# Performance work log

Measured on AMD Instinct MI355X. Metric: run time of the kernel, lower is better.

Reference implementation:

```python
import jax, jax.numpy as jnp
import numpy as np

N = 50000      # nodes
E = 600000     # edges
F_ATOM = 78
D = 128        # hidden_dim = heads * head_dim
H = 8
C = D // H     # 16
ED = 12        # edge_dim
L = 4          # num_layers
B = 512        # graphs in batch
DFF = 4 * D
SCALE = 1.0 / float(np.sqrt(C))


def setup_inputs() -> dict:
    key = jax.random.key(0)
    ks = iter(jax.random.split(key, 128))
    rn = lambda s, sc=0.05: jax.random.normal(next(ks), s, jnp.float32) * sc
    inp = {
        "x": jax.random.normal(next(ks), (N, F_ATOM), jnp.float32),
        "edge_attr": jax.random.normal(next(ks), (E, ED), jnp.float32),
        "edge_index": jax.random.randint(next(ks), (2, E), 0, N),
        "batch": jnp.sort(jax.random.randint(next(ks), (N,), 0, B)),
        "Wemb": rn((F_ATOM, D)), "bemb": jnp.zeros((D,), jnp.float32),
        "Wout": rn((D, D)), "bout": jnp.zeros((D,), jnp.float32),
    }
    def stk(s, sc=0.05):
        return jnp.stack([rn(s, sc) for _ in range(L)])
    inp.update(
        Wq=stk((D, D)), bq=jnp.zeros((L, D), jnp.float32),
        Wk=stk((D, D)), bk=jnp.zeros((L, D), jnp.float32),
        Wv=stk((D, D)), bv=jnp.zeros((L, D), jnp.float32),
        We=stk((ED, D)), be=jnp.zeros((L, D), jnp.float32),
        Wskip=stk((D, D)), bskip=jnp.zeros((L, D), jnp.float32),
        Wbeta=stk((3 * D,)),
        g1=jnp.ones((L, D), jnp.float32), b1=jnp.zeros((L, D), jnp.float32),
        g2=jnp.ones((L, D), jnp.float32), b2=jnp.zeros((L, D), jnp.float32),
        Wf1=stk((D, DFF)), bf1=jnp.zeros((L, DFF), jnp.float32),
        Wf2=stk((DFF, D)), bf2=jnp.zeros((L, D), jnp.float32),
    )
    return inp


def _ln(x, g, b):
    mu = jnp.mean(x, -1, keepdims=True)
    var = jnp.mean((x - mu) ** 2, -1, keepdims=True)
    return (x - mu) * jax.lax.rsqrt(var + 1e-5) * g + b


def _seg_softmax(alpha, dst):
    # alpha: [E, H]; softmax over edges sharing a destination node
    m = jax.ops.segment_max(alpha, dst, num_segments=N)
    m = jnp.where(jnp.isfinite(m), m, 0.0)
    ex = jnp.exp(alpha - m[dst])
    den = jax.ops.segment_sum(ex, dst, num_segments=N)
    return ex / (den[dst] + 1e-16)


def _forward(x, edge_attr, Wemb, bemb, Wq, bq, Wk, bk, Wv, bv, We, be,
             Wskip, bskip, Wbeta, g1, b1, g2, b2, Wf1, bf1, Wf2, bf2,
             Wout, bout, edge_index, batch):
    src, dst = edge_index[0], edge_index[1]
    h = x @ Wemb + bemb                                    # [N, D]
    for l in range(L):
        q = (h @ Wq[l] + bq[l]).reshape(N, H, C)
        k = (h @ Wk[l] + bk[l]).reshape(N, H, C)
        v = (h @ Wv[l] + bv[l]).reshape(N, H, C)
        e = (edge_attr @ We[l] + be[l]).reshape(E, H, C)
        kj = k[src] + e                                    # [E, H, C]
        alpha = jnp.einsum('ehc,ehc->eh', q[dst], kj) * SCALE
        a = _seg_softmax(alpha, dst)                       # [E, H]
        msg = (v[src] + e) * a[:, :, None]                 # [E, H, C]
        agg = jax.ops.segment_sum(msg, dst, num_segments=N).reshape(N, D)
        xr = h @ Wskip[l] + bskip[l]                       # root/skip transform
        beta = jax.nn.sigmoid(
            jnp.concatenate([agg, xr, agg - xr], -1) @ Wbeta[l])[:, None]
        hc = beta * xr + (1.0 - beta) * agg                # beta gate
        h = _ln(hc + h, g1[l], b1[l])
        ff = jax.nn.relu(h @ Wf1[l] + bf1[l]) @ Wf2[l] + bf2[l]
        h = _ln(ff + h, g2[l], b2[l])
    cnt = jax.ops.segment_sum(jnp.ones((N,), h.dtype), batch, num_segments=B)
    pooled = jax.ops.segment_sum(h, batch, num_segments=B) / jnp.maximum(cnt, 1.0)[:, None]
    return pooled @ Wout + bout                            # [B, D]


def reference(x, edge_attr, edge_index, batch, Wemb, bemb, Wout, bout,
              Wq, bq, Wk, bk, Wv, bv, We, be, Wskip, bskip, Wbeta,
              g1, b1, g2, b2, Wf1, bf1, Wf2, bf2):
    return _forward(x, edge_attr, Wemb, bemb, Wq, bq, Wk, bk, Wv, bv, We, be,
                    Wskip, bskip, Wbeta, g1, b1, g2, b2, Wf1, bf1, Wf2, bf2,
                    Wout, bout, edge_index, batch)
```

## Files before the change

### kernel.cpp

```cpp
#include <hip/hip_runtime.h>
#include <math.h>

#define N_NODES 50000
#define N_EDGES 600000
#define FATOM   78
#define DIM     128
#define HEADS   8
#define EDIM    12
#define LAYERS  4
#define NBATCH  512
#define NDFF    512
#define ASCALE  0.25f

typedef __attribute__((ext_vector_type(8))) short bf16x8;
typedef __attribute__((ext_vector_type(4))) float f32x4;

__device__ __forceinline__ float sum16(float v){
  #pragma unroll
  for (int m=1;m<16;m<<=1) v += __shfl_xor(v, m);
  return v;
}
__device__ __forceinline__ float half_sum(float v){
  #pragma unroll
  for (int m=1;m<32;m<<=1) v += __shfl_xor(v, m);
  return v;
}
__device__ __forceinline__ short f2b(float f){
  unsigned int u = __builtin_bit_cast(unsigned int, f);
  u += 0x7fffu + ((u>>16)&1u);
  return (short)(u>>16);
}
__device__ __forceinline__ float b2f_lo(unsigned int u){ return __builtin_bit_cast(float, u<<16); }
__device__ __forceinline__ float b2f_hi(unsigned int u){ return __builtin_bit_cast(float, u & 0xffff0000u); }

__device__ __forceinline__ void gload16(const short* g, short* l){
  __builtin_amdgcn_global_load_lds(
      (const __attribute__((address_space(1))) void*)g,
      (__attribute__((address_space(3))) void*)l, 16, 0, 0);
}

__global__ void count_kernel(const int* __restrict__ ei, int* __restrict__ cnt){
  int e = blockIdx.x*256 + threadIdx.x;
  if (e < N_EDGES) atomicAdd(&cnt[ei[N_EDGES + e]], 1);
}

__global__ __launch_bounds__(1024) void scan1(const int* __restrict__ cnt,
                                              int* __restrict__ row_start, int* __restrict__ bsum){
  __shared__ int lds[1024];
  int gid = blockIdx.x*1024 + threadIdx.x;
  int v = (gid < N_NODES) ? cnt[gid] : 0;
  lds[threadIdx.x] = v; __syncthreads();
  for (int off=1; off<1024; off<<=1){
    int add = (threadIdx.x>=off)?lds[threadIdx.x-off]:0;
    __syncthreads();
    lds[threadIdx.x]+=add;
    __syncthreads();
  }
  if (gid < N_NODES) row_start[gid+1] = lds[threadIdx.x];
  if (threadIdx.x==1023) bsum[blockIdx.x] = lds[1023];
}
__global__ void scan2(int* __restrict__ bsum, int nb){
  int tid = threadIdx.x;
  int v = (tid < nb) ? bsum[tid] : 0;
  #pragma unroll
  for (int off=1; off<64; off<<=1){
    int u = __shfl_up(v, off);
    if (tid >= off) v += u;
  }
  if (tid < nb) bsum[tid] = v;
}
__global__ void scan3(int* __restrict__ row_start, const int* __restrict__ bsum){
  int gid = blockIdx.x*256 + threadIdx.x;
  if (gid == 0) row_start[0] = 0;
  if (gid < N_NODES){
    int blk = gid >> 10;
    if (blk > 0) row_start[gid+1] += bsum[blk-1];
  }
}

__global__ void scatter_kernel(const int* __restrict__ ei, const float* __restrict__ ea,
                               int* __restrict__ cnt2, const int* __restrict__ row_start,
                               int* __restrict__ src_s, short* __restrict__ ea_s){
  int e = blockIdx.x*256 + threadIdx.x;
  if (e < N_EDGES){
    int d = ei[N_EDGES + e];
    int pos = atomicAdd(&cnt2[d], 1);
    int p = row_start[d] + pos;
    src_s[p] = ei[e];
    const float* src = ea + (size_t)e*EDIM;
    unsigned int* dst = (unsigned int*)(ea_s + (size_t)p*EDIM);
    #pragma unroll
    for (int j=0;j<6;j++){
      unsigned int lo = (unsigned int)(unsigned short)f2b(src[2*j]);
      unsigned int hi = (unsigned int)(unsigned short)f2b(src[2*j+1]);
      dst[j] = lo | (hi<<16);
    }
  }
}

__global__ __launch_bounds__(256) void deg_hist(const int* __restrict__ cnt, int* __restrict__ dhist){
  __shared__ int lh[256];
  lh[threadIdx.x] = 0; __syncthreads();
  int n = blockIdx.x*256 + threadIdx.x;
  if (n < N_NODES){
    int d = cnt[n]; if (d > 255) d = 255;
    atomicAdd(&lh[d], 1);
  }
  __syncthreads();
  int c = lh[threadIdx.x];
  if (c) atomicAdd(&dhist[threadIdx.x], c);
}
__global__ __launch_bounds__(256) void deg_scan(const int* __restrict__ dhist, int* __restrict__ dstart){
  __shared__ int l[256];
  int t = threadIdx.x;
  int v = dhist[t];
  l[t] = v; __syncthreads();
  for (int off=1; off<256; off<<=1){
    int add = (t>=off)? l[t-off]:0;
    __syncthreads();
    l[t]+=add;
    __syncthreads();
  }
  dstart[t] = l[t]-v;
}
__global__ __launch_bounds__(256) void deg_place(const int* __restrict__ cnt, int* __restrict__ dcnt,
                                                 const int* __restrict__ dstart, int* __restrict__ perm){
  __shared__ int lh[256];
  __shared__ int lbase[256];
  __shared__ int lrank[256];
  int t = threadIdx.x;
  lh[t] = 0; lrank[t] = 0; __syncthreads();
  int n = blockIdx.x*256 + t;
  int d = -1;
  if (n < N_NODES){
    d = cnt[n]; if (d > 255) d = 255;
    atomicAdd(&lh[d], 1);
  }
  __syncthreads();
  int c = lh[t];
  lbase[t] = c ? atomicAdd(&dcnt[t], c) : 0;
  __syncthreads();
  if (n < N_NODES){
    int r = atomicAdd(&lrank[d], 1);
    perm[dstart[d] + lbase[d] + r] = n;
  }
}

__global__ __launch_bounds__(256) void pack_weights(
  const float* __restrict__ Wq, const float* __restrict__ Wk,
  const float* __restrict__ Wv, const float* __restrict__ Ws,
  const float* __restrict__ bq, const float* __restrict__ bk,
  const float* __restrict__ bv, const float* __restrict__ bs,
  const float* __restrict__ Wf1, const float* __restrict__ Wf2,
  short* __restrict__ wq_t, short* __restrict__ wf1_t, short* __restrict__ wf2_t,
  float* __restrict__ bqkvs)
{
  int l = blockIdx.y;
  int idx = blockIdx.x*256 + threadIdx.x;
  int sec = idx >> 16, r = idx & 65535;
  if (sec == 0){
    int n = r >> 7, k = r & 127;
    const float* W = (n<128)?Wq:(n<256)?Wk:(n<384)?Wv:Ws;
    float v = W[(size_t)l*16384 + k*128 + (n&127)];
    wq_t[(size_t)l*65536 + n*128 + k] = f2b(v);
    if (k == 0){
      const float* bb = (n<128)?bq:(n<256)?bk:(n<384)?bv:bs;
      bqkvs[l*512 + n] = bb[l*128 + (n&127)];
    }
  } else if (sec == 1){
    int n = r >> 7, k = r & 127;
    wf1_t[(size_t)l*65536 + n*128 + k] = f2b(Wf1[(size_t)l*65536 + k*512 + n]);
  } else {
    int n = r >> 9, k = r & 511;
    wf2_t[(size_t)l*65536 + n*512 + k] = f2b(Wf2[(size_t)l*65536 + k*128 + n]);
  }
}

__global__ void pack_emb(const float* __restrict__ Wemb, short* __restrict__ wemb_t){
  int idx = blockIdx.x*256 + threadIdx.x;
  int nn = idx >> 7, k = idx & 127;
  wemb_t[nn*128 + k] = (k < FATOM) ? f2b(Wemb[(size_t)k*DIM + nn]) : (short)0;
}

__global__ void cast_pad_x(const float* __restrict__ x, short* __restrict__ xb){
  int idx = blockIdx.x*256 + threadIdx.x;
  int n = idx >> 6, kp = (idx & 63)*2;
  if (n >= N_NODES) return;
  float v0 = (kp   < FATOM) ? x[(size_t)n*FATOM + kp]   : 0.f;
  float v1 = (kp+1 < FATOM) ? x[(size_t)n*FATOM + kp+1] : 0.f;
  unsigned int lo = (unsigned int)(unsigned short)f2b(v0);
  unsigned int hi = (unsigned int)(unsigned short)f2b(v1);
  *(unsigned int*)(xb + (size_t)n*128 + kp) = lo | (hi<<16);
}

__global__ __launch_bounds__(256) void mfma_gemm(
    const short* __restrict__ A,
    const short* __restrict__ Bt,
    const float* __restrict__ bias,
    float* __restrict__ Cf,
    short* __restrict__ Cb,
    int Nrows, int K, int M, int relu)
{
  __shared__ short As[128*64];
  __shared__ short Bs[128*64];
  int tid  = threadIdx.x;
  int lane = tid & 63;
  int wave = tid >> 6;
  int wr = wave >> 1, wc = wave & 1;
  int bm = blockIdx.x * 128, bn = blockIdx.y * 128;

  f32x4 zero = {0.f,0.f,0.f,0.f};
  f32x4 acc[4][4];
  #pragma unroll
  for (int m=0;m<4;m++)
    #pragma unroll
    for (int n=0;n<4;n++) acc[m][n] = zero;

  int r0 = wave*32;
  for (int k0 = 0; k0 < K; k0 += 64){
    #pragma unroll
    for (int it=0; it<4; ++it){
      int rr = r0 + it*8;
      int r  = rr + (lane>>3);
      int oct = (lane&7) ^ (r&7);
      int gr = bm + r; if (gr >= Nrows) gr = Nrows-1;
      gload16(A  + (size_t)gr*K       + k0 + oct*8, As + rr*64);
      gload16(Bt + (size_t)(bn + r)*K + k0 + oct*8, Bs + rr*64);
    }
    __syncthreads();
    #pragma unroll
    for (int ks=0; ks<2; ++ks){
      bf16x8 af[4], bfv[4];
      #pragma unroll
      for (int m=0;m<4;m++){
        int row = wr*64 + m*16 + (lane&15);
        int oi  = ks*4 + (lane>>4);
        af[m] = *(const bf16x8*)(As + row*64 + ((oi ^ (row&7))<<3));
      }
      #pragma unroll
      for (int n=0;n<4;n++){
        int col = wc*64 + n*16 + (lane&15);
        int oi  = ks*4 + (lane>>4);
        bfv[n] = *(const bf16x8*)(Bs + col*64 + ((oi ^ (col&7))<<3));
      }
      #pragma unroll
      for (int m=0;m<4;m++)
        #pragma unroll
        for (int n=0;n<4;n++)
          acc[m][n] = __builtin_amdgcn_mfma_f32_16x16x32_bf16(af[m], bfv[n], acc[m][n], 0, 0, 0);
    }
    __syncthreads();
  }

  #pragma unroll
  for (int m=0;m<4;m++){
    #pragma unroll
    for (int n=0;n<4;n++){
      int col = bn + wc*64 + n*16 + (lane&15);
      float bval = bias[col];
      #pragma unroll
      for (int j=0;j<4;j++){
        int row = bm + wr*64 + m*16 + (lane>>4)*4 + j;
        if (row < Nrows){
          float v = acc[m][n][j] + bval;
          if (relu) v = fmaxf(v, 0.f);
          if (Cf) Cf[(size_t)row*M + col] = v;
          if (Cb) Cb[(size_t)row*M + col] = f2b(v);
        }
      }
    }
  }
}

__global__ __launch_bounds__(256) void edge_attn_fused(
  const short* __restrict__ qkvx,
  const short* __restrict__ ea_s, const int* __restrict__ src_s,
  const float* __restrict__ Wel, const float* __restrict__ bel,
  const int* __restrict__ row_start, const int* __restrict__ perm,
  float* __restrict__ h, short* __restrict__ hb,
  const float* __restrict__ Wb, const float* __restrict__ g, const float* __restrict__ b)
{
  int wid = (blockIdx.x*256 + threadIdx.x) >> 4;
  if (wid >= N_NODES) return;
  int node = perm[wid];
  int ln = threadIdx.x & 15;
  int c0 = ln*8;

  const short* qrow = qkvx + (size_t)node*512;
  uint4 qu = *(const uint4*)(qrow + c0);
  float q0=b2f_lo(qu.x), q1=b2f_hi(qu.x), q2=b2f_lo(qu.y), q3=b2f_hi(qu.y);
  float q4=b2f_lo(qu.z), q5=b2f_hi(qu.z), q6=b2f_lo(qu.w), q7=b2f_hi(qu.w);

  float u[12];
  #pragma unroll
  for (int j=0;j<12;j++){
    float4 wA = *(const float4*)(Wel + j*DIM + c0);
    float4 wB = *(const float4*)(Wel + j*DIM + c0 + 4);
    float pp = q0*wA.x+q1*wA.y+q2*wA.z+q3*wA.w
             + q4*wB.x+q5*wB.y+q6*wB.z+q7*wB.w;
    u[j] = pp + __shfl_xor(pp,1);
  }
  float4 beA = *(const float4*)(bel + c0);
  float4 beB = *(const float4*)(bel + c0 + 4);
  float qbe;
  { float pp = q0*beA.x+q1*beA.y+q2*beA.z+q3*beA.w
             + q4*beB.x+q5*beB.y+q6*beB.z+q7*beB.w;
    qbe = pp + __shfl_xor(pp,1); }

  int rs = row_start[node], re = row_start[node+1];
  float den = 0.f;
  float av[8] = {0.f,0.f,0.f,0.f,0.f,0.f,0.f,0.f};
  float aEA[12] = {0.f,0.f,0.f,0.f,0.f,0.f,0.f,0.f,0.f,0.f,0.f,0.f};
  for (int i=rs; i<re; ++i){
    int s = src_s[i];
    const short* eap = ea_s + (size_t)i*EDIM;
    uint2 eu0 = *(const uint2*)(eap);
    uint2 eu1 = *(const uint2*)(eap+4);
    uint2 eu2 = *(const uint2*)(eap+8);
    float ea[12];
    ea[0]=b2f_lo(eu0.x); ea[1]=b2f_hi(eu0.x); ea[2]=b2f_lo(eu0.y); ea[3]=b2f_hi(eu0.y);
    ea[4]=b2f_lo(eu1.x); ea[5]=b2f_hi(eu1.x); ea[6]=b2f_lo(eu1.y); ea[7]=b2f_hi(eu1.y);
    ea[8]=b2f_lo(eu2.x); ea[9]=b2f_hi(eu2.x); ea[10]=b2f_lo(eu2.y); ea[11]=b2f_hi(eu2.y);
    const short* srow = qkvx + (size_t)s*512;
    uint4 ku = *(const uint4*)(srow + 128 + c0);
    uint4 vu = *(const uint4*)(srow + 256 + c0);
    float pp = q0*b2f_lo(ku.x) + q1*b2f_hi(ku.x) + q2*b2f_lo(ku.y) + q3*b2f_hi(ku.y)
             + q4*b2f_lo(ku.z) + q5*b2f_hi(ku.z) + q6*b2f_lo(ku.w) + q7*b2f_hi(ku.w);
    float alpha = pp + __shfl_xor(pp,1) + qbe;
    #pragma unroll
    for (int j=0;j<12;j++) alpha += ea[j]*u[j];
    float p = __expf(alpha * ASCALE);
    den += p;
    av[0] += p*b2f_lo(vu.x); av[1] += p*b2f_hi(vu.x);
    av[2] += p*b2f_lo(vu.y); av[3] += p*b2f_hi(vu.y);
    av[4] += p*b2f_lo(vu.z); av[5] += p*b2f_hi(vu.z);
    av[6] += p*b2f_lo(vu.w); av[7] += p*b2f_hi(vu.w);
    #pragma unroll
    for (int j=0;j<12;j++) aEA[j] += p*ea[j];
  }
  float inv = 1.f/(den + 1e-16f);
  float gg[8];
  #pragma unroll
  for (int c=0;c<8;c++) gg[c] = av[c]*inv;
  #pragma unroll
  for (int j=0;j<12;j++){
    float wgt = aEA[j]*inv;
    float4 wA = *(const float4*)(Wel + j*DIM + c0);
    float4 wB = *(const float4*)(Wel + j*DIM + c0 + 4);
    gg[0]+=wgt*wA.x; gg[1]+=wgt*wA.y; gg[2]+=wgt*wA.z; gg[3]+=wgt*wA.w;
    gg[4]+=wgt*wB.x; gg[5]+=wgt*wB.y; gg[6]+=wgt*wB.z; gg[7]+=wgt*wB.w;
  }
  gg[0]+=beA.x; gg[1]+=beA.y; gg[2]+=beA.z; gg[3]+=beA.w;
  gg[4]+=beB.x; gg[5]+=beB.y; gg[6]+=beB.z; gg[7]+=beB.w;

  uint4 xu = *(const uint4*)(qrow + 384 + c0);
  float x[8];
  x[0]=b2f_lo(xu.x); x[1]=b2f_hi(xu.x); x[2]=b2f_lo(xu.y); x[3]=b2f_hi(xu.y);
  x[4]=b2f_lo(xu.z); x[5]=b2f_hi(xu.z); x[6]=b2f_lo(xu.w); x[7]=b2f_hi(xu.w);
  float4 hA = *(const float4*)(h + (size_t)node*DIM + c0);
  float4 hB = *(const float4*)(h + (size_t)node*DIM + c0 + 4);
  float hv[8] = {hA.x,hA.y,hA.z,hA.w,hB.x,hB.y,hB.z,hB.w};
  float4 waA = *(const float4*)(Wb + c0),       waB = *(const float4*)(Wb + c0 + 4);
  float4 wxA = *(const float4*)(Wb + DIM + c0), wxB = *(const float4*)(Wb + DIM + c0 + 4);
  float4 wdA = *(const float4*)(Wb + 2*DIM + c0), wdB = *(const float4*)(Wb + 2*DIM + c0 + 4);
  float wa[8] = {waA.x,waA.y,waA.z,waA.w,waB.x,waB.y,waB.z,waB.w};
  float wx[8] = {wxA.x,wxA.y,wxA.z,wxA.w,wxB.x,wxB.y,wxB.z,wxB.w};
  float wd[8] = {wdA.x,wdA.y,wdA.z,wdA.w,wdB.x,wdB.y,wdB.z,wdB.w};
  float sacc = 0.f;
  #pragma unroll
  for (int c=0;c<8;c++) sacc += gg[c]*wa[c] + x[c]*wx[c] + (gg[c]-x[c])*wd[c];
  sacc = sum16(sacc);
  float beta = 1.f/(1.f + __expf(-sacc));
  float t[8], ts = 0.f;
  #pragma unroll
  for (int c=0;c<8;c++){ t[c] = beta*x[c] + (1.f-beta)*gg[c] + hv[c]; ts += t[c]; }
  float mu = sum16(ts)*(1.f/128.f);
  float vs = 0.f;
  #pragma unroll
  for (int c=0;c<8;c++){ t[c] -= mu; vs += t[c]*t[c]; }
  float var = sum16(vs)*(1.f/128.f);
  float r = rsqrtf(var + 1e-5f);
  float4 gA = *(const float4*)(g + c0), gB = *(const float4*)(g + c0 + 4);
  float4 bA = *(const float4*)(b + c0), bB = *(const float4*)(b + c0 + 4);
  float gv[8] = {gA.x,gA.y,gA.z,gA.w,gB.x,gB.y,gB.z,gB.w};
  float bv[8] = {bA.x,bA.y,bA.z,bA.w,bB.x,bB.y,bB.z,bB.w};
  float o[8];
  #pragma unroll
  for (int c=0;c<8;c++) o[c] = t[c]*r*gv[c] + bv[c];
  float4 oA = {o[0],o[1],o[2],o[3]}, oB = {o[4],o[5],o[6],o[7]};
  *(float4*)(h + (size_t)node*DIM + c0)     = oA;
  *(float4*)(h + (size_t)node*DIM + c0 + 4) = oB;
  uint4 ou;
  ou.x = (unsigned int)(unsigned short)f2b(o[0]) | ((unsigned int)(unsigned short)f2b(o[1])<<16);
  ou.y = (unsigned int)(unsigned short)f2b(o[2]) | ((unsigned int)(unsigned short)f2b(o[3])<<16);
  ou.z = (unsigned int)(unsigned short)f2b(o[4]) | ((unsigned int)(unsigned short)f2b(o[5])<<16);
  ou.w = (unsigned int)(unsigned short)f2b(o[6]) | ((unsigned int)(unsigned short)f2b(o[7])<<16);
  *(uint4*)(hb + (size_t)node*DIM + c0) = ou;
}

__global__ __launch_bounds__(256) void add_ln_kernel(
  const float* __restrict__ t_in, float* __restrict__ h, short* __restrict__ hb,
  const float* __restrict__ g, const float* __restrict__ b)
{
  int wid = (blockIdx.x*256 + threadIdx.x) >> 5;
  if (wid >= N_NODES) return;
  int ln = threadIdx.x & 31;
  int c0 = ln*4;
  float4 t2 = *(const float4*)(t_in + (size_t)wid*DIM + c0);
  float4 h2 = *(const float4*)(h    + (size_t)wid*DIM + c0);
  float t0=t2.x+h2.x, t1=t2.y+h2.y, t3v=t2.z+h2.z, t4=t2.w+h2.w;
  float mu = half_sum(t0+t1+t3v+t4)*(1.f/128.f);
  float d0=t0-mu, d1=t1-mu, d2=t3v-mu, d3=t4-mu;
  float var = half_sum(d0*d0+d1*d1+d2*d2+d3*d3)*(1.f/128.f);
  float r = rsqrtf(var + 1e-5f);
  float4 gv = *(const float4*)(g+c0);
  float4 bv = *(const float4*)(b+c0);
  float o0=d0*r*gv.x+bv.x, o1=d1*r*gv.y+bv.y, o2=d2*r*gv.z+bv.z, o3=d3*r*gv.w+bv.w;
  float4 o; o.x=o0; o.y=o1; o.z=o2; o.w=o3;
  *(float4*)(h + (size_t)wid*DIM + c0) = o;
  unsigned int u0 = (unsigned int)(unsigned short)f2b(o0) | ((unsigned int)(unsigned short)f2b(o1)<<16);
  unsigned int u1 = (unsigned int)(unsigned short)f2b(o2) | ((unsigned int)(unsigned short)f2b(o3)<<16);
  uint2 ou; ou.x=u0; ou.y=u1;
  *(uint2*)(hb + (size_t)wid*DIM + c0) = ou;
}

__global__ __launch_bounds__(128) void pool_out(
  const float* __restrict__ h, const int* __restrict__ batch,
  const float* __restrict__ Wout, const float* __restrict__ bout,
  float* __restrict__ out)
{
  int bidx = blockIdx.x;
  int d = threadIdx.x;
  __shared__ int seg[2];
  __shared__ float p[DIM];
  if (d < 2){
    int target = bidx + d;
    int lo = 0, hi = N_NODES;
    while (lo < hi){ int mid = (lo+hi)>>1; if (batch[mid] < target) lo = mid+1; else hi = mid; }
    seg[d] = lo;
  }
  __syncthreads();
  int lo = seg[0], hi = seg[1];
  float s = 0.f;
  for (int n=lo; n<hi; ++n) s += h[(size_t)n*DIM + d];
  float cnt = (float)(hi - lo);
  p[d] = s / fmaxf(cnt, 1.f);
  __syncthreads();
  float o = bout[d];
  #pragma unroll 8
  for (int kk=0; kk<DIM; ++kk) o += p[kk]*Wout[kk*DIM + d];
  out[bidx*DIM + d] = o;
}

extern "C" void kernel_launch(void* const* d_in, const int* in_sizes, int n_in,
                              void* d_out, int out_size, void* d_ws, size_t ws_size,
                              hipStream_t stream)
{
  const float* x     = (const float*)d_in[0];
  const float* ea    = (const float*)d_in[1];
  const int*   ei    = (const int*)d_in[2];
  const int*   batch = (const int*)d_in[3];
  const float* Wemb  = (const float*)d_in[4];
  const float* bemb  = (const float*)d_in[5];
  const float* Wout  = (const float*)d_in[6];
  const float* bout  = (const float*)d_in[7];
  const float* Wq    = (const float*)d_in[8];
  const float* bq    = (const float*)d_in[9];
  const float* Wk    = (const float*)d_in[10];
  const float* bk    = (const float*)d_in[11];
  const float* Wv    = (const float*)d_in[12];
  const float* bv    = (const float*)d_in[13];
  const float* We    = (const float*)d_in[14];
  const float* be    = (const float*)d_in[15];
  const float* Wskip = (const float*)d_in[16];
  const float* bskip = (const float*)d_in[17];
  const float* Wbeta = (const float*)d_in[18];
  const float* g1    = (const float*)d_in[19];
  const float* b1    = (const float*)d_in[20];
  const float* g2    = (const float*)d_in[21];
  const float* b2    = (const float*)d_in[22];
  const float* Wf1   = (const float*)d_in[23];
  const float* bf1   = (const float*)d_in[24];
  const float* Wf2   = (const float*)d_in[25];
  const float* bf2   = (const float*)d_in[26];
  float* out = (float*)d_out;

  float* ws     = (float*)d_ws;
  float* h      = ws;
  float* ffout  = h + (size_t)N_NODES*DIM;
  float* bqkvs  = ffout + (size_t)N_NODES*DIM;
  short* ea_s   = (short*)(bqkvs + LAYERS*512);
  short* hb     = ea_s + (size_t)N_EDGES*EDIM;
  short* region = hb + (size_t)N_NODES*DIM;
  short* xb     = region + (size_t)N_NODES*NDFF;
  short* wemb_t = xb + (size_t)N_NODES*DIM;
  short* wq_t   = wemb_t + DIM*DIM;
  short* wf1_t  = wq_t  + (size_t)LAYERS*NDFF*DIM;
  short* wf2_t  = wf1_t + (size_t)LAYERS*NDFF*DIM;
  int*   cnt       = (int*)(wf2_t + (size_t)LAYERS*NDFF*DIM);
  int*   cnt2      = cnt + N_NODES;
  int*   row_start = cnt2 + N_NODES;
  int*   bsum      = row_start + N_NODES + 1;
  int*   dhist     = bsum + 64;
  int*   dcnt      = dhist + 256;
  int*   dstart    = dcnt + 256;
  int*   node_perm = dstart + 256;
  int*   src_s     = node_perm + N_NODES;

  hipMemsetAsync(cnt,  0, N_NODES*sizeof(int), stream);
  hipMemsetAsync(cnt2, 0, N_NODES*sizeof(int), stream);
  hipMemsetAsync(dhist, 0, 512*sizeof(int), stream);

  const int NB_SCAN = (N_NODES + 1023)/1024;
  const int NB_DEG  = (N_NODES + 255)/256;
  count_kernel<<<(N_EDGES+255)/256, 256, 0, stream>>>(ei, cnt);
  scan1<<<NB_SCAN, 1024, 0, stream>>>(cnt, row_start, bsum);
  scan2<<<1, 64, 0, stream>>>(bsum, NB_SCAN);
  scan3<<<(N_NODES+255)/256, 256, 0, stream>>>(row_start, bsum);
  deg_hist<<<NB_DEG, 256, 0, stream>>>(cnt, dhist);
  deg_scan<<<1, 256, 0, stream>>>(dhist, dstart);
  deg_place<<<NB_DEG, 256, 0, stream>>>(cnt, dcnt, dstart, node_perm);
  scatter_kernel<<<(N_EDGES+255)/256, 256, 0, stream>>>(ei, ea, cnt2, row_start, src_s, ea_s);

  pack_weights<<<dim3(768, LAYERS), 256, 0, stream>>>(
      Wq, Wk, Wv, Wskip, bq, bk, bv, bskip, Wf1, Wf2, wq_t, wf1_t, wf2_t, bqkvs);
  pack_emb<<<64, 256, 0, stream>>>(Wemb, wemb_t);
  cast_pad_x<<<(N_NODES*64 + 255)/256, 256, 0, stream>>>(x, xb);

  int gM = (N_NODES + 127)/128;
  int attnBlocks = (N_NODES*16 + 255)/256;
  int lnBlocks   = (N_NODES*32 + 255)/256;

  mfma_gemm<<<dim3(gM, 1), 256, 0, stream>>>(xb, wemb_t, bemb, h, hb, N_NODES, DIM, DIM, 0);

  for (int l=0; l<LAYERS; ++l){
    mfma_gemm<<<dim3(gM, 4), 256, 0, stream>>>(
        hb, wq_t + (size_t)l*NDFF*DIM, bqkvs + l*512, nullptr, region,
        N_NODES, DIM, NDFF, 0);

    edge_attn_fused<<<attnBlocks, 256, 0, stream>>>(
        region, ea_s, src_s, We + (size_t)l*EDIM*DIM, be + l*DIM, row_start, node_perm,
        h, hb, Wbeta + l*3*DIM, g1 + l*DIM, b1 + l*DIM);

    mfma_gemm<<<dim3(gM, 4), 256, 0, stream>>>(
        hb, wf1_t + (size_t)l*NDFF*DIM, bf1 + l*NDFF, nullptr, region,
        N_NODES, DIM, NDFF, 1);

    mfma_gemm<<<dim3(gM, 1), 256, 0, stream>>>(
        region, wf2_t + (size_t)l*DIM*NDFF, bf2 + l*DIM, ffout, nullptr,
        N_NODES, NDFF, DIM, 0);

    add_ln_kernel<<<lnBlocks, 256, 0, stream>>>(ffout, h, hb, g2 + l*DIM, b2 + l*DIM);
  }

  pool_out<<<NBATCH, 128, 0, stream>>>(h, batch, Wout, bout, out);
}
```

Baseline: 923.8 us.

## Fuse FF2 GEMM with residual LayerNorm, specialize K=128 GEMM, unroll edge loop

Replaces the FF2 GEMM plus separate add+LayerNorm kernel with one GEMM whose epilogue adds the residual, reduces row statistics across waves through shared memory and writes h/hb directly. This removes the ffout fp32 round trip and one launch per layer. The K=128 GEMMs now load the full K slab into 64KB of LDS in one pass, dropping the K-loop barriers at the cost of occupancy. The edge attention loop is unrolled by two to overlap gather latency. The fused LN uses an E[x^2]-mu^2 variance, which is slightly less numerically stable.

New measurement: 892.1 us. -3.4%, faster.

```diff
diff --git a/kernel.cpp b/kernel.cpp
--- a/kernel.cpp
+++ b/kernel.cpp
@@ -18,11 +18,6 @@
 __device__ __forceinline__ float sum16(float v){
   #pragma unroll
   for (int m=1;m<16;m<<=1) v += __shfl_xor(v, m);
-  return v;
-}
-__device__ __forceinline__ float half_sum(float v){
-  #pragma unroll
-  for (int m=1;m<32;m<<=1) v += __shfl_xor(v, m);
   return v;
 }
 __device__ __forceinline__ short f2b(float f){
@@ -193,21 +188,32 @@
   *(unsigned int*)(xb + (size_t)n*128 + kp) = lo | (hi<<16);
 }
 
-__global__ __launch_bounds__(256) void mfma_gemm(
+__global__ __launch_bounds__(256) void gemm_k128(
     const short* __restrict__ A,
     const short* __restrict__ Bt,
     const float* __restrict__ bias,
     float* __restrict__ Cf,
     short* __restrict__ Cb,
-    int Nrows, int K, int M, int relu)
+    int Nrows, int M, int relu)
 {
-  __shared__ short As[128*64];
-  __shared__ short Bs[128*64];
+  __shared__ short As[128*128];
+  __shared__ short Bs[128*128];
   int tid  = threadIdx.x;
   int lane = tid & 63;
   int wave = tid >> 6;
   int wr = wave >> 1, wc = wave & 1;
   int bm = blockIdx.x * 128, bn = blockIdx.y * 128;
+  int d  = lane & 15;
+  int lr = lane >> 4;
+
+  #pragma unroll
+  for (int it=0; it<8; ++it){
+    int r = wave*32 + it*4 + lr;
+    int oct = (d & 8) | ((d & 7) ^ (r & 7));
+    int gr = bm + r; if (gr >= Nrows) gr = Nrows-1;
+    gload16(A  + (size_t)gr*128       + oct*8, As + (wave*32 + it*4)*128);
+    gload16(Bt + (size_t)(bn + r)*128 + oct*8, Bs + (wave*32 + it*4)*128);
+  }
 
   f32x4 zero = {0.f,0.f,0.f,0.f};
   f32x4 acc[4][4];
@@ -216,40 +222,29 @@
     #pragma unroll
     for (int n=0;n<4;n++) acc[m][n] = zero;
 
-  int r0 = wave*32;
-  for (int k0 = 0; k0 < K; k0 += 64){
-    #pragma unroll
-    for (int it=0; it<4; ++it){
-      int rr = r0 + it*8;
-      int r  = rr + (lane>>3);
-      int oct = (lane&7) ^ (r&7);
-      int gr = bm + r; if (gr >= Nrows) gr = Nrows-1;
-      gload16(A  + (size_t)gr*K       + k0 + oct*8, As + rr*64);
-      gload16(Bt + (size_t)(bn + r)*K + k0 + oct*8, Bs + rr*64);
-    }
-    __syncthreads();
-    #pragma unroll
-    for (int ks=0; ks<2; ++ks){
-      bf16x8 af[4], bfv[4];
-      #pragma unroll
-      for (int m=0;m<4;m++){
-        int row = wr*64 + m*16 + (lane&15);
-        int oi  = ks*4 + (lane>>4);
-        af[m] = *(const bf16x8*)(As + row*64 + ((oi ^ (row&7))<<3));
-      }
-      #pragma unroll
-      for (int n=0;n<4;n++){
-        int col = wc*64 + n*16 + (lane&15);
-        int oi  = ks*4 + (lane>>4);
-        bfv[n] = *(const bf16x8*)(Bs + col*64 + ((oi ^ (col&7))<<3));
-      }
-      #pragma unroll
-      for (int m=0;m<4;m++)
-        #pragma unroll
-        for (int n=0;n<4;n++)
-          acc[m][n] = __builtin_amdgcn_mfma_f32_16x16x32_bf16(af[m], bfv[n], acc[m][n], 0, 0, 0);
-    }
-    __syncthreads();
+  __syncthreads();
+
+  #pragma unroll
+  for (int ks=0; ks<4; ++ks){
+    int oi = ks*4 + (lane>>4);
+    bf16x8 af[4], bfv[4];
+    #pragma unroll
+    for (int m=0;m<4;m++){
+      int row = wr*64 + m*16 + (lane&15);
+      int slot = (oi&8) | ((oi&7) ^ (row&7));
+      af[m] = *(const bf16x8*)(As + row*128 + slot*8);
+    }
+    #pragma unroll
+    for (int n=0;n<4;n++){
+      int col = wc*64 + n*16 + (lane&15);
+      int slot = (oi&8) | ((oi&7) ^ (col&7));
+      bfv[n] = *(const bf16x8*)(Bs + col*128 + slot*8);
+    }
+    #pragma unroll
+    for (int m=0;m<4;m++)
+      #pragma unroll
+      for (int n=0;n<4;n++)
+        acc[m][n] = __builtin_amdgcn_mfma_f32_16x16x32_bf16(af[m], bfv[n], acc[m][n], 0, 0, 0);
   }
 
   #pragma unroll
@@ -266,6 +261,121 @@
           if (relu) v = fmaxf(v, 0.f);
           if (Cf) Cf[(size_t)row*M + col] = v;
           if (Cb) Cb[(size_t)row*M + col] = f2b(v);
+        }
+      }
+    }
+  }
+}
+
+__global__ __launch_bounds__(256) void gemm_ff2_ln(
+    const short* __restrict__ A,
+    const short* __restrict__ Bt,
+    const float* __restrict__ bias,
+    float* __restrict__ h, short* __restrict__ hb,
+    const float* __restrict__ g, const float* __restrict__ b,
+    int Nrows)
+{
+  __shared__ short As[128*64];
+  __shared__ short Bs[128*64];
+  __shared__ float red[2][128][2];
+  int tid  = threadIdx.x;
+  int lane = tid & 63;
+  int wave = tid >> 6;
+  int wr = wave >> 1, wc = wave & 1;
+  int bm = blockIdx.x * 128;
+
+  f32x4 zero = {0.f,0.f,0.f,0.f};
+  f32x4 acc[4][4];
+  #pragma unroll
+  for (int m=0;m<4;m++)
+    #pragma unroll
+    for (int n=0;n<4;n++) acc[m][n] = zero;
+
+  int r0 = wave*32;
+  for (int k0 = 0; k0 < 512; k0 += 64){
+    #pragma unroll
+    for (int it=0; it<4; ++it){
+      int rr = r0 + it*8;
+      int r  = rr + (lane>>3);
+      int oct = (lane&7) ^ (r&7);
+      int gr = bm + r; if (gr >= Nrows) gr = Nrows-1;
+      gload16(A  + (size_t)gr*512 + k0 + oct*8, As + rr*64);
+      gload16(Bt + (size_t)r*512  + k0 + oct*8, Bs + rr*64);
+    }
+    __syncthreads();
+    #pragma unroll
+    for (int ks=0; ks<2; ++ks){
+      bf16x8 af[4], bfv[4];
+      #pragma unroll
+      for (int m=0;m<4;m++){
+        int row = wr*64 + m*16 + (lane&15);
+        int oi  = ks*4 + (lane>>4);
+        af[m] = *(const bf16x8*)(As + row*64 + ((oi ^ (row&7))<<3));
+      }
+      #pragma unroll
+      for (int n=0;n<4;n++){
+        int col = wc*64 + n*16 + (lane&15);
+        int oi  = ks*4 + (lane>>4);
+        bfv[n] = *(const bf16x8*)(Bs + col*64 + ((oi ^ (col&7))<<3));
+      }
+      #pragma unroll
+      for (int m=0;m<4;m++)
+        #pragma unroll
+        for (int n=0;n<4;n++)
+          acc[m][n] = __builtin_amdgcn_mfma_f32_16x16x32_bf16(af[m], bfv[n], acc[m][n], 0, 0, 0);
+    }
+    __syncthreads();
+  }
+
+  #pragma unroll
+  for (int m=0;m<4;m++){
+    #pragma unroll
+    for (int n=0;n<4;n++){
+      int col = wc*64 + n*16 + (lane&15);
+      float bval = bias[col];
+      #pragma unroll
+      for (int j=0;j<4;j++){
+        int row = wr*64 + m*16 + (lane>>4)*4 + j;
+        int grow = bm + row; if (grow >= Nrows) grow = Nrows-1;
+        acc[m][n][j] += bval + h[(size_t)grow*DIM + col];
+      }
+    }
+  }
+  #pragma unroll
+  for (int m=0;m<4;m++){
+    #pragma unroll
+    for (int j=0;j<4;j++){
+      float ps = 0.f, pq = 0.f;
+      #pragma unroll
+      for (int n=0;n<4;n++){ float v = acc[m][n][j]; ps += v; pq += v*v; }
+      #pragma unroll
+      for (int msk=1; msk<16; msk<<=1){ ps += __shfl_xor(ps, msk); pq += __shfl_xor(pq, msk); }
+      if ((lane&15)==0){
+        int row = wr*64 + m*16 + (lane>>4)*4 + j;
+        red[wc][row][0] = ps;
+        red[wc][row][1] = pq;
+      }
+    }
+  }
+  __syncthreads();
+  #pragma unroll
+  for (int m=0;m<4;m++){
+    #pragma unroll
+    for (int j=0;j<4;j++){
+      int row = wr*64 + m*16 + (lane>>4)*4 + j;
+      float S = red[0][row][0] + red[1][row][0];
+      float Q = red[0][row][1] + red[1][row][1];
+      float mu  = S*(1.f/128.f);
+      float var = fmaxf(Q*(1.f/128.f) - mu*mu, 0.f);
+      float rr  = rsqrtf(var + 1e-5f);
+      int grow = bm + row;
+      if (grow < Nrows){
+        #pragma unroll
+        for (int n=0;n<4;n++){
+          int col = wc*64 + n*16 + (lane&15);
+          float o = (acc[m][n][j]-mu)*rr*g[col] + b[col];
+          h[(size_t)grow*DIM + col]  = o;
+          hb[(size_t)grow*DIM + col] = f2b(o);
         }
       }
     }
@@ -311,16 +421,64 @@
   float den = 0.f;
   float av[8] = {0.f,0.f,0.f,0.f,0.f,0.f,0.f,0.f};
   float aEA[12] = {0.f,0.f,0.f,0.f,0.f,0.f,0.f,0.f,0.f,0.f,0.f,0.f};
-  for (int i=rs; i<re; ++i){
+
+  int i = rs;
+  for (; i+2 <= re; i += 2){
+    int s0 = src_s[i], s1 = src_s[i+1];
+    const short* e0p = ea_s + (size_t)i*EDIM;
+    uint2 a00 = *(const uint2*)(e0p);
+    uint2 a01 = *(const uint2*)(e0p+4);
+    uint2 a02 = *(const uint2*)(e0p+8);
+    uint2 a10 = *(const uint2*)(e0p+12);
+    uint2 a11 = *(const uint2*)(e0p+16);
+    uint2 a12 = *(const uint2*)(e0p+20);
+    const short* r0p = qkvx + (size_t)s0*512;
+    const short* r1p = qkvx + (size_t)s1*512;
+    uint4 ku0 = *(const uint4*)(r0p + 128 + c0);
+    uint4 vu0 = *(const uint4*)(r0p + 256 + c0);
+    uint4 ku1 = *(const uint4*)(r1p + 128 + c0);
+    uint4 vu1 = *(const uint4*)(r1p + 256 + c0);
+
+    float ea0[12], ea1[12];
+    ea0[0]=b2f_lo(a00.x); ea0[1]=b2f_hi(a00.x); ea0[2]=b2f_lo(a00.y); ea0[3]=b2f_hi(a00.y);
+    ea0[4]=b2f_lo(a01.x); ea0[5]=b2f_hi(a01.x); ea0[6]=b2f_lo(a01.y); ea0[7]=b2f_hi(a01.y);
+    ea0[8]=b2f_lo(a02.x); ea0[9]=b2f_hi(a02.x); ea0[10]=b2f_lo(a02.y); ea0[11]=b2f_hi(a02.y);
+    ea1[0]=b2f_lo(a10.x); ea1[1]=b2f_hi(a10.x); ea1[2]=b2f_lo(a10.y); ea1[3]=b2f_hi(a10.y);
+    ea1[4]=b2f_lo(a11.x); ea1[5]=b2f_hi(a11.x); ea1[6]=b2f_lo(a11.y); ea1[7]=b2f_hi(a11.y);
+    ea1[8]=b2f_lo(a12.x); ea1[9]=b2f_hi(a12.x); ea1[10]=b2f_lo(a12.y); ea1[11]=b2f_hi(a12.y);
+
+    float pp0 = q0*b2f_lo(ku0.x) + q1*b2f_hi(ku0.x) + q2*b2f_lo(ku0.y) + q3*b2f_hi(ku0.y)
+              + q4*b2f_lo(ku0.z) + q5*b2f_hi(ku0.z) + q6*b2f_lo(ku0.w) + q7*b2f_hi(ku0.w);
+    float pp1 = q0*b2f_lo(ku1.x) + q1*b2f_hi(ku1.x) + q2*b2f_lo(ku1.y) + q3*b2f_hi(ku1.y)
+              + q4*b2f_lo(ku1.z) + q5*b2f_hi(ku1.z) + q6*b2f_lo(ku1.w) + q7*b2f_hi(ku1.w);
+    float al0 = pp0 + __shfl_xor(pp0,1) + qbe;
+    float al1 = pp1 + __shfl_xor(pp1,1) + qbe;
+    #pragma unroll
+    for (int j=0;j<12;j++){ al0 += ea0[j]*u[j]; al1 += ea1[j]*u[j]; }
+    float p0 = __expf(al0 * ASCALE);
+    float p1 = __expf(al1 * ASCALE);
+    den += p0 + p1;
+    av[0] += p0*b2f_lo(vu0.x) + p1*b2f_lo(vu1.x);
+    av[1] += p0*b2f_hi(vu0.x) + p1*b2f_hi(vu1.x);
+    av[2] += p0*b2f_lo(vu0.y) + p1*b2f_lo(vu1.y);
+    av[3] += p0*b2f_hi(vu0.y) + p1*b2f_hi(vu1.y);
+    av[4] += p0*b2f_lo(vu0.z) + p1*b2f_lo(vu1.z);
+    av[5] += p0*b2f_hi(vu0.z) + p1*b2f_hi(vu1.z);
+    av[6] += p0*b2f_lo(vu0.w) + p1*b2f_lo(vu1.w);
+    av[7] += p0*b2f_hi(vu0.w) + p1*b2f_hi(vu1.w);
+    #pragma unroll
+    for (int j=0;j<12;j++) aEA[j] += p0*ea0[j] + p1*ea1[j];
+  }
+  if (i < re){
     int s = src_s[i];
     const short* eap = ea_s + (size_t)i*EDIM;
     uint2 eu0 = *(const uint2*)(eap);
     uint2 eu1 = *(const uint2*)(eap+4);
     uint2 eu2 = *(const uint2*)(eap+8);
-    float ea[12];
-    ea[0]=b2f_lo(eu0.x); ea[1]=b2f_hi(eu0.x); ea[2]=b2f_lo(eu0.y); ea[3]=b2f_hi(eu0.y);
-    ea[4]=b2f_lo(eu1.x); ea[5]=b2f_hi(eu1.x); ea[6]=b2f_lo(eu1.y); ea[7]=b2f_hi(eu1.y);
-    ea[8]=b2f_lo(eu2.x); ea[9]=b2f_hi(eu2.x); ea[10]=b2f_lo(eu2.y); ea[11]=b2f_hi(eu2.y);
+    float ea0[12];
+    ea0[0]=b2f_lo(eu0.x); ea0[1]=b2f_hi(eu0.x); ea0[2]=b2f_lo(eu0.y); ea0[3]=b2f_hi(eu0.y);
+    ea0[4]=b2f_lo(eu1.x); ea0[5]=b2f_hi(eu1.x); ea0[6]=b2f_lo(eu1.y); ea0[7]=b2f_hi(eu1.y);
+    ea0[8]=b2f_lo(eu2.x); ea0[9]=b2f_hi(eu2.x); ea0[10]=b2f_lo(eu2.y); ea0[11]=b2f_hi(eu2.y);
     const short* srow = qkvx + (size_t)s*512;
     uint4 ku = *(const uint4*)(srow + 128 + c0);
     uint4 vu = *(const uint4*)(srow + 256 + c0);
@@ -328,7 +486,7 @@
              + q4*b2f_lo(ku.z) + q5*b2f_hi(ku.z) + q6*b2f_lo(ku.w) + q7*b2f_hi(ku.w);
     float alpha = pp + __shfl_xor(pp,1) + qbe;
     #pragma unroll
-    for (int j=0;j<12;j++) alpha += ea[j]*u[j];
+    for (int j=0;j<12;j++) alpha += ea0[j]*u[j];
     float p = __expf(alpha * ASCALE);
     den += p;
     av[0] += p*b2f_lo(vu.x); av[1] += p*b2f_hi(vu.x);
@@ -336,8 +494,9 @@
     av[4] += p*b2f_lo(vu.z); av[5] += p*b2f_hi(vu.z);
     av[6] += p*b2f_lo(vu.w); av[7] += p*b2f_hi(vu.w);
     #pragma unroll
-    for (int j=0;j<12;j++) aEA[j] += p*ea[j];
-  }
+    for (int j=0;j<12;j++) aEA[j] += p*ea0[j];
+  }
+
   float inv = 1.f/(den + 1e-16f);
   float gg[8];
   #pragma unroll
@@ -396,32 +555,6 @@
   ou.z = (unsigned int)(unsigned short)f2b(o[4]) | ((unsigned int)(unsigned short)f2b(o[5])<<16);
   ou.w = (unsigned int)(unsigned short)f2b(o[6]) | ((unsigned int)(unsigned short)f2b(o[7])<<16);
   *(uint4*)(hb + (size_t)node*DIM + c0) = ou;
-}
-
-__global__ __launch_bounds__(256) void add_ln_kernel(
-  const float* __restrict__ t_in, float* __restrict__ h, short* __restrict__ hb,
-  const float* __restrict__ g, const float* __restrict__ b)
-{
-  int wid = (blockIdx.x*256 + threadIdx.x) >> 5;
-  if (wid >= N_NODES) return;
-  int ln = threadIdx.x & 31;
-  int c0 = ln*4;
-  float4 t2 = *(const float4*)(t_in + (size_t)wid*DIM + c0);
-  float4 h2 = *(const float4*)(h    + (size_t)wid*DIM + c0);
-  float t0=t2.x+h2.x, t1=t2.y+h2.y, t3v=t2.z+h2.z, t4=t2.w+h2.w;
-  float mu = half_sum(t0+t1+t3v+t4)*(1.f/128.f);
-  float d0=t0-mu, d1=t1-mu, d2=t3v-mu, d3=t4-mu;
-  float var = half_sum(d0*d0+d1*d1+d2*d2+d3*d3)*(1.f/128.f);
-  float r = rsqrtf(var + 1e-5f);
-  float4 gv = *(const float4*)(g+c0);
-  float4 bv = *(const float4*)(b+c0);
-  float o0=d0*r*gv.x+bv.x, o1=d1*r*gv.y+bv.y, o2=d2*r*gv.z+bv.z, o3=d3*r*gv.w+bv.w;
-  float4 o; o.x=o0; o.y=o1; o.z=o2; o.w=o3;
-  *(float4*)(h + (size_t)wid*DIM + c0) = o;
-  unsigned int u0 = (unsigned int)(unsigned short)f2b(o0) | ((unsigned int)(unsigned short)f2b(o1)<<16);
-  unsigned int u1 = (unsigned int)(unsigned short)f2b(o2) | ((unsigned int)(unsigned short)f2b(o3)<<16);
-  uint2 ou; ou.x=u0; ou.y=u1;
-  *(uint2*)(hb + (size_t)wid*DIM + c0) = ou;
 }
 
 __global__ __launch_bounds__(128) void pool_out(
@@ -487,8 +620,7 @@
 
   float* ws     = (float*)d_ws;
   float* h      = ws;
-  float* ffout  = h + (size_t)N_NODES*DIM;
-  float* bqkvs  = ffout + (size_t)N_NODES*DIM;
+  float* bqkvs  = h + (size_t)N_NODES*DIM;
   short* ea_s   = (short*)(bqkvs + LAYERS*512);
   short* hb     = ea_s + (size_t)N_EDGES*EDIM;
   short* region = hb + (size_t)N_NODES*DIM;
@@ -529,28 +661,25 @@
 
   int gM = (N_NODES + 127)/128;
   int attnBlocks = (N_NODES*16 + 255)/256;
-  int lnBlocks   = (N_NODES*32 + 255)/256;
-
-  mfma_gemm<<<dim3(gM, 1), 256, 0, stream>>>(xb, wemb_t, bemb, h, hb, N_NODES, DIM, DIM, 0);
+
+  gemm_k128<<<dim3(gM, 1), 256, 0, stream>>>(xb, wemb_t, bemb, h, hb, N_NODES, DIM, 0);
 
   for (int l=0; l<LAYERS; ++l){
-    mfma_gemm<<<dim3(gM, 4), 256, 0, stream>>>(
+    gemm_k128<<<dim3(gM, 4), 256, 0, stream>>>(
         hb, wq_t + (size_t)l*NDFF*DIM, bqkvs + l*512, nullptr, region,
-        N_NODES, DIM, NDFF, 0);
+        N_NODES, NDFF, 0);
 
     edge_attn_fused<<<attnBlocks, 256, 0, stream>>>(
         region, ea_s, src_s, We + (size_t)l*EDIM*DIM, be + l*DIM, row_start, node_perm,
         h, hb, Wbeta + l*3*DIM, g1 + l*DIM, b1 + l*DIM);
 
-    mfma_gemm<<<dim3(gM, 4), 256, 0, stream>>>(
+    gemm_k128<<<dim3(gM, 4), 256, 0, stream>>>(
         hb, wf1_t + (size_t)l*NDFF*DIM, bf1 + l*NDFF, nullptr, region,
-        N_NODES, DIM, NDFF, 1);
-
-    mfma_gemm<<<dim3(gM, 1), 256, 0, stream>>>(
-        region, wf2_t + (size_t)l*DIM*NDFF, bf2 + l*DIM, ffout, nullptr,
-        N_NODES, NDFF, DIM, 0);
-
-    add_ln_kernel<<<lnBlocks, 256, 0, stream>>>(ffout, h, hb, g2 + l*DIM, b2 + l*DIM);
+        N_NODES, NDFF, 1);
+
+    gemm_ff2_ln<<<dim3(gM, 1), 256, 0, stream>>>(
+        region, wf2_t + (size_t)l*DIM*NDFF, bf2 + l*DIM, h, hb,
+        g2 + l*DIM, b2 + l*DIM, N_NODES);
   }
 
   pool_out<<<NBATCH, 128, 0, stream>>>(h, batch, Wout, bout, out);
```
